# Kernel optimization log

Measured on AMD Instinct MI355X. Metric: run time of the kernel, lower is better.

Reference implementation:

```python
import jax, jax.numpy as jnp
import numpy as np

N = 100000       # nodes
E = 1600000      # edges (before self-loops)
IN = 32          # input_dim
HID = 64         # hidden_dim
HEADS = 4
HO = HID // HEADS  # per-head out of gat1
OUT = 32         # output_dim
HID2 = HID // 2
BN_EPS = 1e-5
NEG_SLOPE = 0.2  # PyG GATConv default leaky relu slope


def setup_inputs() -> dict:
    key = jax.random.key(0)
    ks = jax.random.split(key, 28)
    f32 = jnp.float32
    rn = lambda k, s, sc=0.1: jax.random.normal(k, s, f32) * sc
    inp = {}
    inp["x"] = jax.random.normal(ks[0], (N, IN), f32)
    inp["edge_index"] = jax.random.randint(ks[1], (2, E), 0, N, jnp.int32)
    # GATConv 1: in=IN, heads=HEADS, out/head=HO, concat
    inp["W1"] = rn(ks[2], (IN, HEADS * HO))
    inp["att_src1"] = rn(ks[3], (HEADS, HO))
    inp["att_dst1"] = rn(ks[4], (HEADS, HO))
    inp["b1"] = rn(ks[5], (HEADS * HO,))
    # GATConv 2: in=HID, heads=1, out=OUT, no concat (mean)
    inp["W2"] = rn(ks[6], (HID, OUT))
    inp["att_src2"] = rn(ks[7], (1, OUT))
    inp["att_dst2"] = rn(ks[8], (1, OUT))
    inp["b2"] = rn(ks[9], (OUT,))
    # BatchNorms (inference mode: running stats)
    inp["bn1_g"] = jnp.ones((HID,), f32)
    inp["bn1_b"] = jnp.zeros((HID,), f32)
    inp["bn1_m"] = rn(ks[10], (HID,), 0.1)
    inp["bn1_v"] = jax.random.uniform(ks[11], (HID,), f32, 0.5, 1.5)
    inp["bn2_g"] = jnp.ones((OUT,), f32)
    inp["bn2_b"] = jnp.zeros((OUT,), f32)
    inp["bn2_m"] = rn(ks[12], (OUT,), 0.1)
    inp["bn2_v"] = jax.random.uniform(ks[13], (OUT,), f32, 0.5, 1.5)
    # classifier: OUT -> HID2 -> 3
    inp["cls_w1"] = rn(ks[14], (OUT, HID2))
    inp["cls_b1"] = rn(ks[15], (HID2,))
    inp["cls_w2"] = rn(ks[16], (HID2, 3))
    inp["cls_b2"] = rn(ks[17], (3,))
    inp["reg_w1"] = rn(ks[18], (OUT, HID2))
    inp["reg_b1"] = rn(ks[19], (HID2,))
    inp["reg_w2"] = rn(ks[20], (HID2, 1))
    inp["reg_b2"] = rn(ks[21], (1,))
    return inp


def _segment_softmax(e, seg, n):
    # e: [E, H]; softmax over edges sharing the same destination segment
    m = jax.ops.segment_max(e, seg, num_segments=n)
    ex = jnp.exp(e - m[seg])
    s = jax.ops.segment_sum(ex, seg, num_segments=n)
    return ex / (s[seg] + 1e-16)


def _gat(x, src, dst, W, a_src, a_dst, b, heads, ho, concat):
    n = x.shape[0]
    h = (x @ W).reshape(n, heads, ho)                    # [N,H,F]
    e = (h * a_src).sum(-1)[src] + (h * a_dst).sum(-1)[dst]  # [E,H]
    e = jax.nn.leaky_relu(e, NEG_SLOPE)
    alpha = _segment_softmax(e, dst, n)                  # [E,H]
    out = jax.ops.segment_sum(h[src] * alpha[:, :, None], dst, num_segments=n)
    out = out.reshape(n, heads * ho) if concat else out.mean(axis=1)
    return out + b


def _bn(x, g, b, m, v):
    return (x - m) * jax.lax.rsqrt(v + BN_EPS) * g + b


def reference(x, edge_index, W1, att_src1, att_dst1, b1, W2, att_src2, att_dst2, b2,
              bn1_g, bn1_b, bn1_m, bn1_v, bn2_g, bn2_b, bn2_m, bn2_v,
              cls_w1, cls_b1, cls_w2, cls_b2, reg_w1, reg_b1, reg_w2, reg_b2):
    n = x.shape[0]
    # PyG GATConv default add_self_loops=True
    loops = jnp.arange(n, dtype=edge_index.dtype)
    src = jnp.concatenate([edge_index[0], loops])
    dst = jnp.concatenate([edge_index[1], loops])

    h = _gat(x, src, dst, W1, att_src1, att_dst1, b1, HEADS, HO, True)   # [N, HID]
    h = jax.nn.relu(_bn(h, bn1_g, bn1_b, bn1_m, bn1_v))
    emb = _gat(h, src, dst, W2, att_src2, att_dst2, b2, 1, OUT, False)   # [N, OUT]
    emb = jax.nn.relu(_bn(emb, bn2_g, bn2_b, bn2_m, bn2_v))

    roles = jax.nn.relu(emb @ cls_w1 + cls_b1) @ cls_w2 + cls_b2          # [N, 3]
    energy = jax.nn.relu(emb @ reg_w1 + reg_b1) @ reg_w2 + reg_b2         # [N, 1]
    return emb, roles, energy
```

## Files before the change

kernel.cpp:

```cpp
#include <hip/hip_runtime.h>
#include <hip/hip_bf16.h>

#define NN 100000
#define EE 1600000
#define ETOT (EE + NN)
#define IND 32
#define HIDD 64
#define NHEADS 4
#define OUTD 32
#define HID2D 32
#define LOG2E 1.44269504f

#define BSH 8
#define NBUCK 391
#define CAP 5120
#define EPB 8192

typedef unsigned int uint;

__device__ __forceinline__ uint pack2(float a, float b) {
  uint lo = (uint)__bfloat16_as_ushort(__float2bfloat16(a));
  uint hi = (uint)__bfloat16_as_ushort(__float2bfloat16(b));
  return (hi << 16) | lo;
}
__device__ __forceinline__ float lo2f(uint w) { return __uint_as_float(w << 16); }
__device__ __forceinline__ float hi2r(uint w) { return __uint_as_float(w); }

__global__ __launch_bounds__(256) void k_lin1(
    const float* __restrict__ x, const float* __restrict__ W1,
    const float* __restrict__ atsrc, const float* __restrict__ atdst,
    uint* __restrict__ h1u, float* __restrict__ as1, float* __restrict__ ad1) {
  __shared__ float Ws[IND * HIDD];
  __shared__ float xs[8 * IND];
  __shared__ float atS[HIDD], atD[HIDD];
  int t = threadIdx.x;
  for (int i = t; i < IND * HIDD; i += 256) Ws[i] = W1[i];
  if (t < HIDD) { atS[t] = atsrc[t]; atD[t] = atdst[t]; }
  xs[t] = x[blockIdx.x * 256 + t];
  __syncthreads();
  int nl = t >> 5, tl = t & 31;
  int node = blockIdx.x * 8 + nl;
  int j0 = 2 * tl, j1 = j0 + 1;
  float a0 = 0.f, a1 = 0.f;
#pragma unroll
  for (int k = 0; k < IND; k++) {
    float xv = xs[nl * IND + k];
    a0 += xv * Ws[k * HIDD + j0];
    a1 += xv * Ws[k * HIDD + j1];
  }
  h1u[node * 32 + tl] = pack2(a0, a1);
  float ps = a0 * atS[j0] + a1 * atS[j1];
  float pd = a0 * atD[j0] + a1 * atD[j1];
#pragma unroll
  for (int off = 4; off >= 1; off >>= 1) {
    ps += __shfl_down(ps, off, 8);
    pd += __shfl_down(pd, off, 8);
  }
  if ((tl & 7) == 0) {
    as1[node * NHEADS + (tl >> 3)] = ps * LOG2E;
    ad1[node * NHEADS + (tl >> 3)] = pd * LOG2E;
  }
}

__global__ __launch_bounds__(256) void k_lin2(
    const float* __restrict__ hbn, const float* __restrict__ W2,
    const float* __restrict__ atsrc, const float* __restrict__ atdst,
    uint* __restrict__ h2u, float* __restrict__ as2, float* __restrict__ ad2) {
  __shared__ float Ws[HIDD * OUTD];
  __shared__ float xs[16 * HIDD];
  __shared__ float atS[OUTD], atD[OUTD];
  int t = threadIdx.x;
  for (int i = t; i < HIDD * OUTD; i += 256) Ws[i] = W2[i];
  if (t < OUTD) { atS[t] = atsrc[t]; atD[t] = atdst[t]; }
  for (int i = t; i < 16 * HIDD; i += 256) xs[i] = hbn[blockIdx.x * 16 * HIDD + i];
  __syncthreads();
  int nl = t >> 4, tl = t & 15;
  int node = blockIdx.x * 16 + nl;
  int j0 = 2 * tl, j1 = j0 + 1;
  float a0 = 0.f, a1 = 0.f;
#pragma unroll
  for (int k = 0; k < HIDD; k++) {
    float xv = xs[nl * HIDD + k];
    a0 += xv * Ws[k * OUTD + j0];
    a1 += xv * Ws[k * OUTD + j1];
  }
  h2u[node * 16 + tl] = pack2(a0, a1);
  float ps = a0 * atS[j0] + a1 * atS[j1];
  float pd = a0 * atD[j0] + a1 * atD[j1];
#pragma unroll
  for (int off = 8; off >= 1; off >>= 1) {
    ps += __shfl_down(ps, off, 16);
    pd += __shfl_down(pd, off, 16);
  }
  if (tl == 0) { as2[node] = ps * LOG2E; ad2[node] = pd * LOG2E; }
}

__global__ __launch_bounds__(256) void k_bin(const int* __restrict__ ei,
                                             int* __restrict__ bcur,
                                             int* __restrict__ bins) {
  __shared__ int cnt[NBUCK];
  int t = threadIdx.x;
  for (int i = t; i < NBUCK; i += 256) cnt[i] = 0;
  __syncthreads();
  int base = blockIdx.x * EPB;
  int lim = base + EPB; if (lim > ETOT) lim = ETOT;
  for (int i = base + t; i < lim; i += 256) {
    int d = (i < EE) ? ei[EE + i] : (i - EE);
    atomicAdd(&cnt[d >> BSH], 1);
  }
  __syncthreads();
  for (int i = t; i < NBUCK; i += 256) cnt[i] = atomicAdd(&bcur[i], cnt[i]);
  __syncthreads();
  for (int i = base + t; i < lim; i += 256) {
    int s, d;
    if (i < EE) { s = ei[i]; d = ei[EE + i]; } else { s = i - EE; d = s; }
    int bk = d >> BSH;
    int pos = atomicAdd(&cnt[bk], 1);
    bins[bk * CAP + pos] = (s << BSH) | (d & ((1 << BSH) - 1));
  }
}

__global__ __launch_bounds__(256) void k_csr(const int* __restrict__ bcur,
                                             const int* __restrict__ bins,
                                             int* __restrict__ rowp,
                                             int* __restrict__ srcs) {
  __shared__ int lrec[CAP];
  __shared__ int sA[512], sB[512];
  __shared__ int ldeg[256];
  int b = blockIdx.x, t = threadIdx.x;
  if (b == 0 && t == 0) rowp[NN] = ETOT;
  sA[t] = (t < NBUCK) ? bcur[t] : 0;
  sA[t + 256] = (t + 256 < NBUCK) ? bcur[t + 256] : 0;
  __syncthreads();
  int* in = sA; int* out = sB;
  for (int off = 1; off < 512; off <<= 1) {
    for (int i = t; i < 512; i += 256)
      out[i] = in[i] + ((i >= off) ? in[i - off] : 0);
    __syncthreads();
    int* tmp = in; in = out; out = tmp;
  }
  int gb = (b == 0) ? 0 : in[b - 1];
  __syncthreads();
  int count = bcur[b]; if (count > CAP) count = CAP;
  ldeg[t] = 0;
  __syncthreads();
  for (int i = t; i < count; i += 256) {
    int r = bins[b * CAP + i];
    lrec[i] = r;
    atomicAdd(&ldeg[r & 255], 1);
  }
  __syncthreads();
  int dv = ldeg[t];
  sA[t] = dv;
  __syncthreads();
  in = sA; out = sB;
  for (int off = 1; off < 256; off <<= 1) {
    out[t] = in[t] + ((t >= off) ? in[t - off] : 0);
    __syncthreads();
    int* tmp = in; in = out; out = tmp;
  }
  int nb = b << BSH;
  int ex = in[t] - dv;
  if (nb + t < NN) rowp[nb + t] = gb + ex;
  ldeg[t] = ex;
  __syncthreads();
  for (int i = t; i < count; i += 256) {
    int r = lrec[i];
    int pos = atomicAdd(&ldeg[r & 255], 1);
    srcs[gb + pos] = (r >> BSH) << 3;
  }
}

__global__ __launch_bounds__(256, 4) void k_agg1(
    const int* __restrict__ rowp, const int* __restrict__ srcs,
    const uint* __restrict__ h1u, const float* __restrict__ as1,
    const float* __restrict__ ad1, const float* __restrict__ b1,
    const float* __restrict__ g, const float* __restrict__ bb,
    const float* __restrict__ m, const float* __restrict__ v,
    float* __restrict__ hbn) {
  int t = threadIdx.x;
  int wid = t >> 6, lane = t & 63;
  int nA = blockIdx.x * 8 + wid * 2;
  int nB = nA + 1;
  int slot = lane >> 3;
  int fl = lane & 7;
  int hd = fl >> 1;
  int stA = rowp[nA], eA = rowp[nA + 1], eB = rowp[nB + 1];
  int stB = eA;
  int lpA = eA - 1, lpB = eB - 1;
  float advA = ad1[nA * NHEADS + hd];
  float advB = ad1[nB * NHEADS + hd];
  const uint4* h14 = (const uint4*)h1u;
  float accA[8] = {0,0,0,0,0,0,0,0}, accB[8] = {0,0,0,0,0,0,0,0};
  float lA = 0.f, lB = 0.f;
  int pA = stA + slot, pB = stB + slot;
  int sA0 = srcs[pA < lpA ? pA : lpA];
  int sB0 = srcs[pB < lpB ? pB : lpB];
  uint4 wA = h14[sA0 + fl];
  uint4 wB = h14[sB0 + fl];
  float asA = as1[(sA0 >> 1) + hd];
  float asB = as1[(sB0 >> 1) + hd];
  int p1A = pA + 8, p1B = pB + 8;
  int sA1 = srcs[p1A < lpA ? p1A : lpA];
  int sB1 = srcs[p1B < lpB ? p1B : lpB];
  while (pA < eA || pB < eB) {
    uint4 wnA = h14[sA1 + fl];
    uint4 wnB = h14[sB1 + fl];
    float anA = as1[(sA1 >> 1) + hd];
    float anB = as1[(sB1 >> 1) + hd];
    int p2A = p1A + 8, p2B = p1B + 8;
    int sA2 = srcs[p2A < lpA ? p2A : lpA];
    int sB2 = srcs[p2B < lpB ? p2B : lpB];
    if (pA < eA) {
      float e = asA + advA;
      e = fmaxf(e, 0.2f * e);
      float ex = exp2f(e);
      lA += ex;
      accA[0] += ex * lo2f(wA.x); accA[1] += ex * hi2r(wA.x);
      accA[2] += ex * lo2f(wA.y); accA[3] += ex * hi2r(wA.y);
      accA[4] += ex * lo2f(wA.z); accA[5] += ex * hi2r(wA.z);
      accA[6] += ex * lo2f(wA.w); accA[7] += ex * hi2r(wA.w);
    }
    if (pB < eB) {
      float e = asB + advB;
      e = fmaxf(e, 0.2f * e);
      float ex = exp2f(e);
      lB += ex;
      accB[0] += ex * lo2f(wB.x); accB[1] += ex * hi2r(wB.x);
      accB[2] += ex * lo2f(wB.y); accB[3] += ex * hi2r(wB.y);
      accB[4] += ex * lo2f(wB.z); accB[5] += ex * hi2r(wB.z);
      accB[6] += ex * lo2f(wB.w); accB[7] += ex * hi2r(wB.w);
    }
    wA = wnA; wB = wnB; asA = anA; asB = anB;
    sA1 = sA2; sB1 = sB2;
    pA = p1A; pB = p1B; p1A = p2A; p1B = p2B;
  }
#pragma unroll
  for (int off = 8; off <= 32; off <<= 1) {
#pragma unroll
    for (int i = 0; i < 8; i++) {
      accA[i] += __shfl_xor(accA[i], off, 64);
      accB[i] += __shfl_xor(accB[i], off, 64);
    }
    lA += __shfl_xor(lA, off, 64);
    lB += __shfl_xor(lB, off, 64);
  }
  if (slot < 2) {
    int node = slot == 0 ? nA : nB;
    float lsum = slot == 0 ? lA : lB;
    float li = 1.f / (lsum + 1e-16f);
    int fb = fl * 8;
    float o[8];
#pragma unroll
    for (int i = 0; i < 8; i++) {
      int j = fb + i;
      float av = slot == 0 ? accA[i] : accB[i];
      float ov = av * li + b1[j];
      ov = (ov - m[j]) * rsqrtf(v[j] + 1e-5f) * g[j] + bb[j];
      o[i] = fmaxf(ov, 0.f);
    }
    float4* dst = (float4*)(hbn + node * HIDD + fb);
    dst[0] = make_float4(o[0], o[1], o[2], o[3]);
    dst[1] = make_float4(o[4], o[5], o[6], o[7]);
  }
}

__global__ __launch_bounds__(256, 4) void k_agg2(
    const int* __restrict__ rowp, const int* __restrict__ srcs,
    const uint* __restrict__ h2u, const float* __restrict__ as2,
    const float* __restrict__ ad2, const float* __restrict__ b2v,
    const float* __restrict__ g, const float* __restrict__ bb,
    const float* __restrict__ m, const float* __restrict__ v,
    float* __restrict__ out_emb) {
  int t = threadIdx.x;
  int wid = t >> 6, lane = t & 63;
  int nA = blockIdx.x * 8 + wid * 2;
  int nB = nA + 1;
  int slot = lane >> 3;
  int fl = lane & 7;
  int stA = rowp[nA], eA = rowp[nA + 1], eB = rowp[nB + 1];
  int stB = eA;
  int lpA = eA - 1, lpB = eB - 1;
  float advA = ad2[nA], advB = ad2[nB];
  const uint2* h22 = (const uint2*)h2u;
  float accA[4] = {0,0,0,0}, accB[4] = {0,0,0,0};
  float lA = 0.f, lB = 0.f;
  int pA = stA + slot, pB = stB + slot;
  int sA0 = srcs[pA < lpA ? pA : lpA];
  int sB0 = srcs[pB < lpB ? pB : lpB];
  uint2 wA = h22[sA0 + fl];
  uint2 wB = h22[sB0 + fl];
  float asA = as2[sA0 >> 3], asB = as2[sB0 >> 3];
  int p1A = pA + 8, p1B = pB + 8;
  int sA1 = srcs[p1A < lpA ? p1A : lpA];
  int sB1 = srcs[p1B < lpB ? p1B : lpB];
  while (pA < eA || pB < eB) {
    uint2 wnA = h22[sA1 + fl];
    uint2 wnB = h22[sB1 + fl];
    float anA = as2[sA1 >> 3], anB = as2[sB1 >> 3];
    int p2A = p1A + 8, p2B = p1B + 8;
    int sA2 = srcs[p2A < lpA ? p2A : lpA];
    int sB2 = srcs[p2B < lpB ? p2B : lpB];
    if (pA < eA) {
      float e = asA + advA;
      e = fmaxf(e, 0.2f * e);
      float ex = exp2f(e);
      lA += ex;
      accA[0] += ex * lo2f(wA.x); accA[1] += ex * hi2r(wA.x);
      accA[2] += ex * lo2f(wA.y); accA[3] += ex * hi2r(wA.y);
    }
    if (pB < eB) {
      float e = asB + advB;
      e = fmaxf(e, 0.2f * e);
      float ex = exp2f(e);
      lB += ex;
      accB[0] += ex * lo2f(wB.x); accB[1] += ex * hi2r(wB.x);
      accB[2] += ex * lo2f(wB.y); accB[3] += ex * hi2r(wB.y);
    }
    wA = wnA; wB = wnB; asA = anA; asB = anB;
    sA1 = sA2; sB1 = sB2;
    pA = p1A; pB = p1B; p1A = p2A; p1B = p2B;
  }
#pragma unroll
  for (int off = 8; off <= 32; off <<= 1) {
#pragma unroll
    for (int i = 0; i < 4; i++) {
      accA[i] += __shfl_xor(accA[i], off, 64);
      accB[i] += __shfl_xor(accB[i], off, 64);
    }
    lA += __shfl_xor(lA, off, 64);
    lB += __shfl_xor(lB, off, 64);
  }
  if (slot < 2) {
    int node = slot == 0 ? nA : nB;
    float lsum = slot == 0 ? lA : lB;
    float li = 1.f / (lsum + 1e-16f);
    int fb = fl * 4;
    float o[4];
#pragma unroll
    for (int i = 0; i < 4; i++) {
      int j = fb + i;
      float av = slot == 0 ? accA[i] : accB[i];
      float ov = av * li + b2v[j];
      ov = (ov - m[j]) * rsqrtf(v[j] + 1e-5f) * g[j] + bb[j];
      o[i] = fmaxf(ov, 0.f);
    }
    *(float4*)(out_emb + node * OUTD + fb) = make_float4(o[0], o[1], o[2], o[3]);
  }
}

__global__ __launch_bounds__(256) void k_mlp(
    const float* __restrict__ embf,
    const float* __restrict__ cw1, const float* __restrict__ cb1,
    const float* __restrict__ cw2, const float* __restrict__ cb2,
    const float* __restrict__ rw1, const float* __restrict__ rb1,
    const float* __restrict__ rw2, const float* __restrict__ rb2,
    float* __restrict__ out_roles, float* __restrict__ out_energy) {
  __shared__ float C1[OUTD * HID2D], R1[OUTD * HID2D];
  __shared__ float C2[HID2D * 3], CB1[HID2D], RB1[HID2D], R2[HID2D];
  __shared__ float CB2v[3], RB2v;
  int t = threadIdx.x;
  for (int i = t; i < OUTD * HID2D; i += 256) { C1[i] = cw1[i]; R1[i] = rw1[i]; }
  if (t < HID2D) { CB1[t] = cb1[t]; RB1[t] = rb1[t]; R2[t] = rw2[t]; }
  if (t < HID2D * 3) C2[t] = cw2[t];
  if (t < 3) CB2v[t] = cb2[t];
  if (t == 0) RB2v = rb2[0];
  __syncthreads();
  int node = blockIdx.x * 256 + t;
  if (node >= NN) return;
  float e[OUTD];
#pragma unroll
  for (int k = 0; k < OUTD; k++) e[k] = embf[node * OUTD + k];
  float r0 = CB2v[0], r1 = CB2v[1], r2 = CB2v[2], en = RB2v;
  for (int j = 0; j < HID2D; j++) {
    float hc = CB1[j], hr = RB1[j];
#pragma unroll
    for (int k = 0; k < OUTD; k++) {
      hc += e[k] * C1[k * HID2D + j];
      hr += e[k] * R1[k * HID2D + j];
    }
    hc = fmaxf(hc, 0.f);
    hr = fmaxf(hr, 0.f);
    r0 += hc * C2[j * 3 + 0];
    r1 += hc * C2[j * 3 + 1];
    r2 += hc * C2[j * 3 + 2];
    en += hr * R2[j];
  }
  out_roles[node * 3 + 0] = r0;
  out_roles[node * 3 + 1] = r1;
  out_roles[node * 3 + 2] = r2;
  out_energy[node] = en;
}

extern "C" void kernel_launch(void* const* d_in, const int* in_sizes, int n_in,
                              void* d_out, int out_size, void* d_ws, size_t ws_size,
                              hipStream_t stream) {
  const float* x    = (const float*)d_in[0];
  const int*   ei   = (const int*)d_in[1];
  const float* W1   = (const float*)d_in[2];
  const float* as1w = (const float*)d_in[3];
  const float* ad1w = (const float*)d_in[4];
  const float* b1   = (const float*)d_in[5];
  const float* W2   = (const float*)d_in[6];
  const float* as2w = (const float*)d_in[7];
  const float* ad2w = (const float*)d_in[8];
  const float* b2v  = (const float*)d_in[9];
  const float* bn1g = (const float*)d_in[10];
  const float* bn1b = (const float*)d_in[11];
  const float* bn1m = (const float*)d_in[12];
  const float* bn1v = (const float*)d_in[13];
  const float* bn2g = (const float*)d_in[14];
  const float* bn2b = (const float*)d_in[15];
  const float* bn2m = (const float*)d_in[16];
  const float* bn2v = (const float*)d_in[17];
  const float* cw1  = (const float*)d_in[18];
  const float* cb1  = (const float*)d_in[19];
  const float* cw2  = (const float*)d_in[20];
  const float* cb2  = (const float*)d_in[21];
  const float* rw1  = (const float*)d_in[22];
  const float* rb1  = (const float*)d_in[23];
  const float* rw2  = (const float*)d_in[24];
  const float* rb2  = (const float*)d_in[25];

  uint*  h1u = (uint*)d_ws;
  float* hbn = (float*)(h1u + NN * 32);
  float* as1 = hbn + NN * HIDD;
  float* ad1 = as1 + NN * NHEADS;
  int* rowp  = (int*)(ad1 + NN * NHEADS);
  int* srcs  = rowp + NN + 1;
  int* bcur  = srcs + ETOT;
  int* bins  = bcur + 512;
  uint* h2u  = h1u;
  float* as2 = as1;
  float* ad2 = ad1;

  float* out        = (float*)d_out;
  float* out_emb    = out;
  float* out_roles  = out + NN * OUTD;
  float* out_energy = out + NN * (OUTD + 3);

  hipMemsetAsync(bcur, 0, 512 * sizeof(int), stream);
  k_lin1<<<NN / 8, 256, 0, stream>>>(x, W1, as1w, ad1w, h1u, as1, ad1);
  k_bin<<<(ETOT + EPB - 1) / EPB, 256, 0, stream>>>(ei, bcur, bins);
  k_csr<<<NBUCK, 256, 0, stream>>>(bcur, bins, rowp, srcs);
  k_agg1<<<NN / 8, 256, 0, stream>>>(rowp, srcs, h1u, as1, ad1, b1, bn1g, bn1b, bn1m, bn1v, hbn);
  k_lin2<<<NN / 16, 256, 0, stream>>>(hbn, W2, as2w, ad2w, h2u, as2, ad2);
  k_agg2<<<NN / 8, 256, 0, stream>>>(rowp, srcs, h2u, as2, ad2, b2v, bn2g, bn2b, bn2m, bn2v, out_emb);
  k_mlp<<<(NN + 255) / 256, 256, 0, stream>>>(out_emb, cw1, cb1, cw2, cb2, rw1, rb1, rw2, rb2, out_roles, out_energy);
}
```

Measured before the change: 319.1 us.

## Aggregate four nodes per wavefront and fold bucket-counter reset into lin1

Each wavefront in both GAT aggregation kernels now processes four destination nodes at once instead of two. This gives more independent gather loads in flight per loop iteration, and the grid is halved to match. The hipMemsetAsync of the bucket counters is removed; block 0 of k_lin1 now zeroes them, saving one operation on the stream. The cost is higher register pressure from 4x8 accumulators under launch_bounds(256,4), and imbalance when the four nodes have different degrees.

```diff
diff --git a/kernel.cpp b/kernel.cpp
--- a/kernel.cpp
+++ b/kernel.cpp
@@ -29,11 +29,13 @@
 __global__ __launch_bounds__(256) void k_lin1(
     const float* __restrict__ x, const float* __restrict__ W1,
     const float* __restrict__ atsrc, const float* __restrict__ atdst,
-    uint* __restrict__ h1u, float* __restrict__ as1, float* __restrict__ ad1) {
+    uint* __restrict__ h1u, float* __restrict__ as1, float* __restrict__ ad1,
+    int* __restrict__ bcur) {
   __shared__ float Ws[IND * HIDD];
   __shared__ float xs[8 * IND];
   __shared__ float atS[HIDD], atD[HIDD];
   int t = threadIdx.x;
+  if (blockIdx.x == 0) { bcur[t] = 0; bcur[t + 256] = 0; }
   for (int i = t; i < IND * HIDD; i += 256) Ws[i] = W1[i];
   if (t < HIDD) { atS[t] = atsrc[t]; atD[t] = atdst[t]; }
   xs[t] = x[blockIdx.x * 256 + t];
@@ -180,82 +182,89 @@
     float* __restrict__ hbn) {
   int t = threadIdx.x;
   int wid = t >> 6, lane = t & 63;
-  int nA = blockIdx.x * 8 + wid * 2;
-  int nB = nA + 1;
+  int n0 = blockIdx.x * 16 + wid * 4;
   int slot = lane >> 3;
   int fl = lane & 7;
   int hd = fl >> 1;
-  int stA = rowp[nA], eA = rowp[nA + 1], eB = rowp[nB + 1];
-  int stB = eA;
-  int lpA = eA - 1, lpB = eB - 1;
-  float advA = ad1[nA * NHEADS + hd];
-  float advB = ad1[nB * NHEADS + hd];
+  int rp[5];
+#pragma unroll
+  for (int k = 0; k < 5; k++) rp[k] = rowp[n0 + k];
   const uint4* h14 = (const uint4*)h1u;
-  float accA[8] = {0,0,0,0,0,0,0,0}, accB[8] = {0,0,0,0,0,0,0,0};
-  float lA = 0.f, lB = 0.f;
-  int pA = stA + slot, pB = stB + slot;
-  int sA0 = srcs[pA < lpA ? pA : lpA];
-  int sB0 = srcs[pB < lpB ? pB : lpB];
-  uint4 wA = h14[sA0 + fl];
-  uint4 wB = h14[sB0 + fl];
-  float asA = as1[(sA0 >> 1) + hd];
-  float asB = as1[(sB0 >> 1) + hd];
-  int p1A = pA + 8, p1B = pB + 8;
-  int sA1 = srcs[p1A < lpA ? p1A : lpA];
-  int sB1 = srcs[p1B < lpB ? p1B : lpB];
-  while (pA < eA || pB < eB) {
-    uint4 wnA = h14[sA1 + fl];
-    uint4 wnB = h14[sB1 + fl];
-    float anA = as1[(sA1 >> 1) + hd];
-    float anB = as1[(sB1 >> 1) + hd];
-    int p2A = p1A + 8, p2B = p1B + 8;
-    int sA2 = srcs[p2A < lpA ? p2A : lpA];
-    int sB2 = srcs[p2B < lpB ? p2B : lpB];
-    if (pA < eA) {
-      float e = asA + advA;
-      e = fmaxf(e, 0.2f * e);
-      float ex = exp2f(e);
-      lA += ex;
-      accA[0] += ex * lo2f(wA.x); accA[1] += ex * hi2r(wA.x);
-      accA[2] += ex * lo2f(wA.y); accA[3] += ex * hi2r(wA.y);
-      accA[4] += ex * lo2f(wA.z); accA[5] += ex * hi2r(wA.z);
-      accA[6] += ex * lo2f(wA.w); accA[7] += ex * hi2r(wA.w);
-    }
-    if (pB < eB) {
-      float e = asB + advB;
-      e = fmaxf(e, 0.2f * e);
-      float ex = exp2f(e);
-      lB += ex;
-      accB[0] += ex * lo2f(wB.x); accB[1] += ex * hi2r(wB.x);
-      accB[2] += ex * lo2f(wB.y); accB[3] += ex * hi2r(wB.y);
-      accB[4] += ex * lo2f(wB.z); accB[5] += ex * hi2r(wB.z);
-      accB[6] += ex * lo2f(wB.w); accB[7] += ex * hi2r(wB.w);
-    }
-    wA = wnA; wB = wnB; asA = anA; asB = anB;
-    sA1 = sA2; sB1 = sB2;
-    pA = p1A; pB = p1B; p1A = p2A; p1B = p2B;
+  float acc[4][8], l[4], adv[4], as[4];
+  int p[4], p1[4], lp[4], en[4], s1v[4];
+  uint4 w[4];
+#pragma unroll
+  for (int k = 0; k < 4; k++) {
+    adv[k] = ad1[(n0 + k) * NHEADS + hd];
+    en[k] = rp[k + 1];
+    lp[k] = en[k] - 1;
+    p[k] = rp[k] + slot;
+    int pc = p[k] < lp[k] ? p[k] : lp[k];
+    int s0 = srcs[pc];
+    w[k] = h14[s0 + fl];
+    as[k] = as1[(s0 >> 1) + hd];
+    p1[k] = p[k] + 8;
+    int pc1 = p1[k] < lp[k] ? p1[k] : lp[k];
+    s1v[k] = srcs[pc1];
+    l[k] = 0.f;
+#pragma unroll
+    for (int i = 0; i < 8; i++) acc[k][i] = 0.f;
+  }
+  while (p[0] < en[0] || p[1] < en[1] || p[2] < en[2] || p[3] < en[3]) {
+    uint4 wn[4]; float an[4]; int s2[4];
+#pragma unroll
+    for (int k = 0; k < 4; k++) {
+      wn[k] = h14[s1v[k] + fl];
+      an[k] = as1[(s1v[k] >> 1) + hd];
+      int p2 = p1[k] + 8;
+      int pc = p2 < lp[k] ? p2 : lp[k];
+      s2[k] = srcs[pc];
+    }
+#pragma unroll
+    for (int k = 0; k < 4; k++) {
+      if (p[k] < en[k]) {
+        float e = as[k] + adv[k];
+        e = fmaxf(e, 0.2f * e);
+        float ex = exp2f(e);
+        l[k] += ex;
+        acc[k][0] += ex * lo2f(w[k].x); acc[k][1] += ex * hi2r(w[k].x);
+        acc[k][2] += ex * lo2f(w[k].y); acc[k][3] += ex * hi2r(w[k].y);
+        acc[k][4] += ex * lo2f(w[k].z); acc[k][5] += ex * hi2r(w[k].z);
+        acc[k][6] += ex * lo2f(w[k].w); acc[k][7] += ex * hi2r(w[k].w);
+      }
+      w[k] = wn[k]; as[k] = an[k]; s1v[k] = s2[k];
+      p[k] = p1[k]; p1[k] += 8;
+    }
   }
 #pragma unroll
   for (int off = 8; off <= 32; off <<= 1) {
 #pragma unroll
-    for (int i = 0; i < 8; i++) {
-      accA[i] += __shfl_xor(accA[i], off, 64);
-      accB[i] += __shfl_xor(accB[i], off, 64);
-    }
-    lA += __shfl_xor(lA, off, 64);
-    lB += __shfl_xor(lB, off, 64);
-  }
-  if (slot < 2) {
-    int node = slot == 0 ? nA : nB;
-    float lsum = slot == 0 ? lA : lB;
+    for (int k = 0; k < 4; k++) {
+#pragma unroll
+      for (int i = 0; i < 8; i++) acc[k][i] += __shfl_xor(acc[k][i], off, 64);
+      l[k] += __shfl_xor(l[k], off, 64);
+    }
+  }
+  if (slot < 4) {
+    float lsum = 0.f, av[8];
+#pragma unroll
+    for (int i = 0; i < 8; i++) av[i] = 0.f;
+#pragma unroll
+    for (int k = 0; k < 4; k++) {
+      if (slot == k) {
+        lsum = l[k];
+#pragma unroll
+        for (int i = 0; i < 8; i++) av[i] = acc[k][i];
+      }
+    }
+    int node = n0 + slot;
     float li = 1.f / (lsum + 1e-16f);
     int fb = fl * 8;
     float o[8];
 #pragma unroll
     for (int i = 0; i < 8; i++) {
       int j = fb + i;
-      float av = slot == 0 ? accA[i] : accB[i];
-      float ov = av * li + b1[j];
+      float ov = av[i] * li + b1[j];
       ov = (ov - m[j]) * rsqrtf(v[j] + 1e-5f) * g[j] + bb[j];
       o[i] = fmaxf(ov, 0.f);
     }
@@ -274,74 +283,86 @@
     float* __restrict__ out_emb) {
   int t = threadIdx.x;
   int wid = t >> 6, lane = t & 63;
-  int nA = blockIdx.x * 8 + wid * 2;
-  int nB = nA + 1;
+  int n0 = blockIdx.x * 16 + wid * 4;
   int slot = lane >> 3;
   int fl = lane & 7;
-  int stA = rowp[nA], eA = rowp[nA + 1], eB = rowp[nB + 1];
-  int stB = eA;
-  int lpA = eA - 1, lpB = eB - 1;
-  float advA = ad2[nA], advB = ad2[nB];
+  int rp[5];
+#pragma unroll
+  for (int k = 0; k < 5; k++) rp[k] = rowp[n0 + k];
   const uint2* h22 = (const uint2*)h2u;
-  float accA[4] = {0,0,0,0}, accB[4] = {0,0,0,0};
-  float lA = 0.f, lB = 0.f;
-  int pA = stA + slot, pB = stB + slot;
-  int sA0 = srcs[pA < lpA ? pA : lpA];
-  int sB0 = srcs[pB < lpB ? pB : lpB];
-  uint2 wA = h22[sA0 + fl];
-  uint2 wB = h22[sB0 + fl];
-  float asA = as2[sA0 >> 3], asB = as2[sB0 >> 3];
-  int p1A = pA + 8, p1B = pB + 8;
-  int sA1 = srcs[p1A < lpA ? p1A : lpA];
-  int sB1 = srcs[p1B < lpB ? p1B : lpB];
-  while (pA < eA || pB < eB) {
-    uint2 wnA = h22[sA1 + fl];
-    uint2 wnB = h22[sB1 + fl];
-    float anA = as2[sA1 >> 3], anB = as2[sB1 >> 3];
-    int p2A = p1A + 8, p2B = p1B + 8;
-    int sA2 = srcs[p2A < lpA ? p2A : lpA];
-    int sB2 = srcs[p2B < lpB ? p2B : lpB];
-    if (pA < eA) {
-      float e = asA + advA;
-      e = fmaxf(e, 0.2f * e);
-      float ex = exp2f(e);
-      lA += ex;
-      accA[0] += ex * lo2f(wA.x); accA[1] += ex * hi2r(wA.x);
-      accA[2] += ex * lo2f(wA.y); accA[3] += ex * hi2r(wA.y);
-    }
-    if (pB < eB) {
-      float e = asB + advB;
-      e = fmaxf(e, 0.2f * e);
-      float ex = exp2f(e);
-      lB += ex;
-      accB[0] += ex * lo2f(wB.x); accB[1] += ex * hi2r(wB.x);
-      accB[2] += ex * lo2f(wB.y); accB[3] += ex * hi2r(wB.y);
-    }
-    wA = wnA; wB = wnB; asA = anA; asB = anB;
-    sA1 = sA2; sB1 = sB2;
-    pA = p1A; pB = p1B; p1A = p2A; p1B = p2B;
+  float acc[4][4], l[4], adv[4], as[4];
+  int p[4], p1[4], lp[4], en[4], s1v[4];
+  uint2 w[4];
+#pragma unroll
+  for (int k = 0; k < 4; k++) {
+    adv[k] = ad2[n0 + k];
+    en[k] = rp[k + 1];
+    lp[k] = en[k] - 1;
+    p[k] = rp[k] + slot;
+    int pc = p[k] < lp[k] ? p[k] : lp[k];
+    int s0 = srcs[pc];
+    w[k] = h22[s0 + fl];
+    as[k] = as2[s0 >> 3];
+    p1[k] = p[k] + 8;
+    int pc1 = p1[k] < lp[k] ? p1[k] : lp[k];
+    s1v[k] = srcs[pc1];
+    l[k] = 0.f;
+#pragma unroll
+    for (int i = 0; i < 4; i++) acc[k][i] = 0.f;
+  }
+  while (p[0] < en[0] || p[1] < en[1] || p[2] < en[2] || p[3] < en[3]) {
+    uint2 wn[4]; float an[4]; int s2[4];
+#pragma unroll
+    for (int k = 0; k < 4; k++) {
+      wn[k] = h22[s1v[k] + fl];
+      an[k] = as2[s1v[k] >> 3];
+      int p2 = p1[k] + 8;
+      int pc = p2 < lp[k] ? p2 : lp[k];
+      s2[k] = srcs[pc];
+    }
+#pragma unroll
+    for (int k = 0; k < 4; k++) {
+      if (p[k] < en[k]) {
+        float e = as[k] + adv[k];
+        e = fmaxf(e, 0.2f * e);
+        float ex = exp2f(e);
+        l[k] += ex;
+        acc[k][0] += ex * lo2f(w[k].x); acc[k][1] += ex * hi2r(w[k].x);
+        acc[k][2] += ex * lo2f(w[k].y); acc[k][3] += ex * hi2r(w[k].y);
+      }
+      w[k] = wn[k]; as[k] = an[k]; s1v[k] = s2[k];
+      p[k] = p1[k]; p1[k] += 8;
+    }
   }
 #pragma unroll
   for (int off = 8; off <= 32; off <<= 1) {
 #pragma unroll
-    for (int i = 0; i < 4; i++) {
-      accA[i] += __shfl_xor(accA[i], off, 64);
-      accB[i] += __shfl_xor(accB[i], off, 64);
-    }
-    lA += __shfl_xor(lA, off, 64);
-    lB += __shfl_xor(lB, off, 64);
-  }
-  if (slot < 2) {
-    int node = slot == 0 ? nA : nB;
-    float lsum = slot == 0 ? lA : lB;
+    for (int k = 0; k < 4; k++) {
+#pragma unroll
+      for (int i = 0; i < 4; i++) acc[k][i] += __shfl_xor(acc[k][i], off, 64);
+      l[k] += __shfl_xor(l[k], off, 64);
+    }
+  }
+  if (slot < 4) {
+    float lsum = 0.f, av[4];
+#pragma unroll
+    for (int i = 0; i < 4; i++) av[i] = 0.f;
+#pragma unroll
+    for (int k = 0; k < 4; k++) {
+      if (slot == k) {
+        lsum = l[k];
+#pragma unroll
+        for (int i = 0; i < 4; i++) av[i] = acc[k][i];
+      }
+    }
+    int node = n0 + slot;
     float li = 1.f / (lsum + 1e-16f);
     int fb = fl * 4;
     float o[4];
 #pragma unroll
     for (int i = 0; i < 4; i++) {
       int j = fb + i;
-      float av = slot == 0 ? accA[i] : accB[i];
-      float ov = av * li + b2v[j];
+      float ov = av[i] * li + b2v[j];
       ov = (ov - m[j]) * rsqrtf(v[j] + 1e-5f) * g[j] + bb[j];
       o[i] = fmaxf(ov, 0.f);
     }
@@ -439,12 +460,11 @@
   float* out_roles  = out + NN * OUTD;
   float* out_energy = out + NN * (OUTD + 3);
 
-  hipMemsetAsync(bcur, 0, 512 * sizeof(int), stream);
-  k_lin1<<<NN / 8, 256, 0, stream>>>(x, W1, as1w, ad1w, h1u, as1, ad1);
+  k_lin1<<<NN / 8, 256, 0, stream>>>(x, W1, as1w, ad1w, h1u, as1, ad1, bcur);
   k_bin<<<(ETOT + EPB - 1) / EPB, 256, 0, stream>>>(ei, bcur, bins);
   k_csr<<<NBUCK, 256, 0, stream>>>(bcur, bins, rowp, srcs);
-  k_agg1<<<NN / 8, 256, 0, stream>>>(rowp, srcs, h1u, as1, ad1, b1, bn1g, bn1b, bn1m, bn1v, hbn);
+  k_agg1<<<NN / 16, 256, 0, stream>>>(rowp, srcs, h1u, as1, ad1, b1, bn1g, bn1b, bn1m, bn1v, hbn);
   k_lin2<<<NN / 16, 256, 0, stream>>>(hbn, W2, as2w, ad2w, h2u, as2, ad2);
-  k_agg2<<<NN / 8, 256, 0, stream>>>(rowp, srcs, h2u, as2, ad2, b2v, bn2g, bn2b, bn2m, bn2v, out_emb);
+  k_agg2<<<NN / 16, 256, 0, stream>>>(rowp, srcs, h2u, as2, ad2, b2v, bn2g, bn2b, bn2m, bn2v, out_emb);
   k_mlp<<<(NN + 255) / 256, 256, 0, stream>>>(out_emb, cw1, cb1, cw2, cb2, rw1, rb1, rw2, rb2, out_roles, out_energy);
 }
```

Result: no change. 315.2 us (-1.2%).
